# Kernel tuning notes

Hardware: AMD Instinct MI355X
Metric: run time of the kernel (lower is better)

Reference implementation:

```python
import jax, jax.numpy as jnp
import numpy as np

NEG_SLOPE = 0.2
EPS = 1e-16


def gat_conv(x, edge_index, W, att_src, att_dst, bias, heads, out_ch, concat):
    """PyG-style GATConv (eval mode, add_self_loops=True)."""
    N = x.shape[0]
    h = (x @ W).reshape(N, heads, out_ch)              # [N,H,C]
    loop = jnp.arange(N, dtype=edge_index.dtype)
    src = jnp.concatenate([edge_index[0], loop])       # [E+N]
    dst = jnp.concatenate([edge_index[1], loop])
    a_src = jnp.sum(h * att_src, axis=-1)              # [N,H]
    a_dst = jnp.sum(h * att_dst, axis=-1)
    e = jax.nn.leaky_relu(a_src[src] + a_dst[dst], NEG_SLOPE)  # [E+N,H]
    # segment softmax over destination nodes
    m = jax.ops.segment_max(e, dst, num_segments=N)
    e = jnp.exp(e - m[dst])
    s = jax.ops.segment_sum(e, dst, num_segments=N)
    alpha = e / (s[dst] + EPS)                         # [E+N,H]
    msg = h[src] * alpha[..., None]                    # [E+N,H,C]
    out = jax.ops.segment_sum(msg, dst, num_segments=N)  # [N,H,C]
    out = out.reshape(N, heads * out_ch) if concat else out.mean(axis=1)
    return out + bias


def setup_inputs() -> dict:
    key = jax.random.key(0)
    ks = jax.random.split(key, 11)
    N, F, E = 100000, 128, 1600000
    H1, C1 = 4, 16
    H2, C2 = 1, 16
    return {
        "x": jax.random.normal(ks[0], (N, F), dtype=jnp.float32),
        "edge_index": jax.random.randint(ks[1], (2, E), 0, N, dtype=jnp.int64) if jax.config.jax_enable_x64 else jax.random.randint(ks[1], (2, E), 0, N).astype(jnp.int32),
        "W1": jax.random.normal(ks[2], (F, H1 * C1), dtype=jnp.float32) * 0.1,
        "att_src1": jax.random.normal(ks[3], (H1, C1), dtype=jnp.float32) * 0.1,
        "att_dst1": jax.random.normal(ks[4], (H1, C1), dtype=jnp.float32) * 0.1,
        "bias1": jax.random.normal(ks[5], (H1 * C1,), dtype=jnp.float32) * 0.1,
        "W2": jax.random.normal(ks[6], (H1 * C1, H2 * C2), dtype=jnp.float32) * 0.1,
        "att_src2": jax.random.normal(ks[7], (H2, C2), dtype=jnp.float32) * 0.1,
        "att_dst2": jax.random.normal(ks[8], (H2, C2), dtype=jnp.float32) * 0.1,
        "bias2": jax.random.normal(ks[9], (C2,), dtype=jnp.float32) * 0.1,
    }


def reference(x, edge_index, W1, att_src1, att_dst1, bias1, W2, att_src2, att_dst2, bias2):
    # dropout is identity in eval mode
    h = gat_conv(x, edge_index, W1, att_src1, att_dst1, bias1, heads=4, out_ch=16, concat=True)
    h = jax.nn.elu(h)
    h = gat_conv(h, edge_index, W2, att_src2, att_dst2, bias2, heads=1, out_ch=16, concat=False)
    return jax.nn.log_softmax(h, axis=1)
```

## Files before the change

kernel.cpp:

```cpp
#include <hip/hip_runtime.h>
#include <hip/hip_fp16.h>
#include <hip/hip_bf16.h>
#include <math.h>


#define BSH 8
#define BCAP 5120
#define CHK 4096

typedef __attribute__((ext_vector_type(8))) short short8;
typedef __attribute__((ext_vector_type(8))) _Float16 half8;
typedef __attribute__((ext_vector_type(4))) _Float16 half4;
typedef __attribute__((ext_vector_type(4))) float float4v;

static __device__ __forceinline__ short f2bf(float f) {
    __hip_bfloat16 b = __float2bfloat16(f);
    return *reinterpret_cast<short*>(&b);
}

__global__ __launch_bounds__(256) void k_pre(const int* __restrict__ ei, int* __restrict__ cursor,
                                             int* __restrict__ stage, int E, int NBK,
                                             const float* __restrict__ x,
                                             const float* __restrict__ W1,
                                             const float* __restrict__ att_src1,
                                             const float* __restrict__ att_dst1,
                                             __half* __restrict__ h1,
                                             float* __restrict__ a_src, float* __restrict__ a_dst,
                                             int N, int GS) {
    __shared__ __align__(16) char smem[80 * 136 * 2];
    int tid = threadIdx.x;
    if (blockIdx.x < GS) {
        int* hist = (int*)smem;
        int* cnt2 = hist + 512;
        int* base = cnt2 + 512;
        int e0 = blockIdx.x * CHK;
        int nedge = E - e0; if (nedge > CHK) nedge = CHK;
        int nv4 = nedge >> 2, rem = nedge & 3;
        const int4* dv4 = (const int4*)(ei + E + e0);
        const int4* sv4 = (const int4*)(ei + e0);
        for (int i = tid; i < 512; i += 256) { hist[i] = 0; cnt2[i] = 0; }
        __syncthreads();
        for (int i = tid; i < nv4; i += 256) {
            int4 d = dv4[i];
            atomicAdd(&hist[d.x >> BSH], 1);
            atomicAdd(&hist[d.y >> BSH], 1);
            atomicAdd(&hist[d.z >> BSH], 1);
            atomicAdd(&hist[d.w >> BSH], 1);
        }
        if (tid < rem) atomicAdd(&hist[ei[E + e0 + nv4 * 4 + tid] >> BSH], 1);
        __syncthreads();
        for (int b = tid; b < NBK; b += 256) {
            int c = hist[b];
            if (c > 0) base[b] = b * BCAP + atomicAdd(&cursor[b], c);
        }
        __syncthreads();
        for (int i = tid; i < nv4; i += 256) {
            int4 s = sv4[i];
            int4 d = dv4[i];
            int b, r;
            b = d.x >> BSH; r = atomicAdd(&cnt2[b], 1);
            stage[base[b] + r] = s.x | ((d.x & 255) << 17);
            b = d.y >> BSH; r = atomicAdd(&cnt2[b], 1);
            stage[base[b] + r] = s.y | ((d.y & 255) << 17);
            b = d.z >> BSH; r = atomicAdd(&cnt2[b], 1);
            stage[base[b] + r] = s.z | ((d.z & 255) << 17);
            b = d.w >> BSH; r = atomicAdd(&cnt2[b], 1);
            stage[base[b] + r] = s.w | ((d.w & 255) << 17);
        }
        if (tid < rem) {
            int e = nv4 * 4 + tid;
            int s = ei[e0 + e];
            int d = ei[E + e0 + e];
            int b = d >> BSH;
            int r = atomicAdd(&cnt2[b], 1);
            stage[base[b] + r] = s | ((d & 255) << 17);
        }
    } else {
        short* wt = (short*)smem;
        for (int i = tid; i < 128 * 64; i += 256) {
            int k = i >> 6, c = i & 63;
            wt[c * 136 + k] = f2bf(W1[i]);
        }
        for (int i = tid; i < 16 * 128; i += 256) {
            int col = i >> 7, k = i & 127;
            float v = 0.f;
            if (col < 8) {
                int h = col & 3;
                const float* att = (col < 4) ? att_src1 : att_dst1;
                #pragma unroll
                for (int c = 0; c < 16; c++) v += W1[k * 64 + h * 16 + c] * att[h * 16 + c];
            }
            wt[(64 + col) * 136 + k] = f2bf(v);
        }
        __syncthreads();
        int wave = tid >> 6, lane = tid & 63;
        int m = lane & 15, q = lane >> 4;
        int nbase = (blockIdx.x - GS) * 64 + wave * 16;
        int anode = nbase + m;
        bool rowok = anode < N;
        const float* xrow = x + (size_t)(rowok ? anode : 0) * 128 + q * 8;

        float4v acc[5];
        #pragma unroll
        for (int ct = 0; ct < 5; ct++)
            #pragma unroll
            for (int r = 0; r < 4; r++) acc[ct][r] = 0.f;

        #pragma unroll
        for (int kc = 0; kc < 4; kc++) {
            float4 u0 = make_float4(0.f, 0.f, 0.f, 0.f), u1 = u0;
            if (rowok) {
                u0 = *(const float4*)(xrow + kc * 32);
                u1 = *(const float4*)(xrow + kc * 32 + 4);
            }
            short8 af;
            af[0] = f2bf(u0.x); af[1] = f2bf(u0.y); af[2] = f2bf(u0.z); af[3] = f2bf(u0.w);
            af[4] = f2bf(u1.x); af[5] = f2bf(u1.y); af[6] = f2bf(u1.z); af[7] = f2bf(u1.w);
            #pragma unroll
            for (int ct = 0; ct < 5; ct++) {
                short8 bf = *(const short8*)&wt[(ct * 16 + m) * 136 + kc * 32 + q * 8];
                acc[ct] = __builtin_amdgcn_mfma_f32_16x16x32_bf16(af, bf, acc[ct], 0, 0, 0);
            }
        }
        #pragma unroll
        for (int ct = 0; ct < 4; ct++) {
            #pragma unroll
            for (int r = 0; r < 4; r++) {
                int n = nbase + q * 4 + r;
                if (n < N) h1[(size_t)n * 64 + ct * 16 + m] = __float2half(acc[ct][r]);
            }
        }
        #pragma unroll
        for (int r = 0; r < 4; r++) {
            int n = nbase + q * 4 + r;
            if (n < N) {
                float v = acc[4][r];
                if (m < 4) a_src[n * 4 + m] = v;
                else if (m < 8) a_dst[n * 4 + (m - 4)] = v;
            }
        }
    }
}

__global__ __launch_bounds__(256) void k_build2(const int* __restrict__ stage,
                                                const int* __restrict__ cursor,
                                                int* __restrict__ row_start,
                                                int* __restrict__ csr,
                                                int NBK, int E, int N) {
    __shared__ int cnt[128];
    __shared__ int lb[128];
    __shared__ int cur[128];
    __shared__ int sA[256];
    int blk = blockIdx.x, tid = threadIdx.x;
    int b = blk >> 1, half = blk & 1;
    int nodes0 = (b << BSH) + (half << 7);
    int nnodes = N - nodes0;
    if (nnodes > 128) nnodes = 128;
    if (nnodes < 0) nnodes = 0;
    int partial = 0;
    for (int i = tid; i < b; i += 256) partial += cursor[i];
    sA[tid] = partial;
    __syncthreads();
    for (int off = 128; off >= 1; off >>= 1) {
        if (tid < off) sA[tid] += sA[tid + off];
        __syncthreads();
    }
    int ebase = sA[0];
    int ecnt = cursor[b];
    __syncthreads();
    if (b == 0 && half == 0 && tid == 0) row_start[N] = E + N;
    const int* sbk = stage + b * BCAP;
    if (tid < 128) cnt[tid] = (tid < nnodes) ? 1 : 0;
    __syncthreads();
    int hb = half << 7;
    int e4 = ecnt & ~3;
    for (int e = tid * 4; e < e4; e += 1024) {
        int4 v = *(const int4*)&sbk[e];
        int l;
        l = (v.x >> 17) & 255; if ((l & 128) == hb) atomicAdd(&cnt[l & 127], 1);
        l = (v.y >> 17) & 255; if ((l & 128) == hb) atomicAdd(&cnt[l & 127], 1);
        l = (v.z >> 17) & 255; if ((l & 128) == hb) atomicAdd(&cnt[l & 127], 1);
        l = (v.w >> 17) & 255; if ((l & 128) == hb) atomicAdd(&cnt[l & 127], 1);
    }
    if (tid < (ecnt & 3)) {
        int l = (sbk[e4 + tid] >> 17) & 255;
        if ((l & 128) == hb) atomicAdd(&cnt[l & 127], 1);
    }
    __syncthreads();
    int myc = (tid < 128) ? cnt[tid] : 0;
    sA[tid] = myc;
    __syncthreads();
    for (int off = 1; off < 128; off <<= 1) {
        int r = sA[tid] + ((tid >= off) ? sA[tid - off] : 0);
        __syncthreads();
        sA[tid] = r;
        __syncthreads();
    }
    int own_width = sA[127];
    int own_edges = own_width - nnodes;
    int half0_edges = half ? (ecnt - own_edges) : 0;
    int gb = ebase + half0_edges + nodes0;
    if (tid < 128) {
        lb[tid] = sA[tid] - myc;
        cur[tid] = 1;
    }
    __syncthreads();
    if (tid < nnodes) {
        row_start[nodes0 + tid] = gb + lb[tid];
        csr[gb + lb[tid]] = nodes0 + tid;
    }
    __syncthreads();
    for (int e = tid * 4; e < e4; e += 1024) {
        int4 v = *(const int4*)&sbk[e];
        int l, r;
        l = (v.x >> 17) & 255;
        if ((l & 128) == hb) { r = atomicAdd(&cur[l & 127], 1); csr[gb + lb[l & 127] + r] = v.x & 0x1FFFF; }
        l = (v.y >> 17) & 255;
        if ((l & 128) == hb) { r = atomicAdd(&cur[l & 127], 1); csr[gb + lb[l & 127] + r] = v.y & 0x1FFFF; }
        l = (v.z >> 17) & 255;
        if ((l & 128) == hb) { r = atomicAdd(&cur[l & 127], 1); csr[gb + lb[l & 127] + r] = v.z & 0x1FFFF; }
        l = (v.w >> 17) & 255;
        if ((l & 128) == hb) { r = atomicAdd(&cur[l & 127], 1); csr[gb + lb[l & 127] + r] = v.w & 0x1FFFF; }
    }
    if (tid < (ecnt & 3)) {
        int v = sbk[e4 + tid];
        int l = (v >> 17) & 255;
        if ((l & 128) == hb) {
            int r = atomicAdd(&cur[l & 127], 1);
            csr[gb + lb[l & 127] + r] = v & 0x1FFFF;
        }
    }
}

__global__ __launch_bounds__(256) void k_agg1f(const int* __restrict__ row_start,
                                               const int* __restrict__ csr_src,
                                               const float* __restrict__ a_src,
                                               const float* __restrict__ a_dst,
                                               const __half* __restrict__ h1,
                                               const float* __restrict__ bias,
                                               const float* __restrict__ W2,
                                               const float* __restrict__ att_src2,
                                               const float* __restrict__ att_dst2,
                                               __half* __restrict__ h2,
                                               float* __restrict__ a_src2,
                                               float* __restrict__ a_dst2, int N) {
    __shared__ float sW2[64 * 17];
    __shared__ float sAs[16], sAd[16];
    int tid = threadIdx.x;
    for (int i = tid; i < 1024; i += 256) sW2[(i >> 4) * 17 + (i & 15)] = W2[i];
    if (tid < 16) { sAs[tid] = att_src2[tid]; sAd[tid] = att_dst2[tid]; }
    __syncthreads();
    int wave = tid >> 6, lane = tid & 63;
    int grp = lane >> 3, sub = lane & 3, par = (lane >> 2) & 1;
    int node = blockIdx.x * 32 + wave * 8 + grp;
    if (node >= N) return;
    int row = row_start[node];
    int deg = row_start[node + 1] - row;
    float adm = a_dst[node * 4 + sub];
    const _Float16* hb = (const _Float16*)h1 + sub * 16;
    const int* cp = csr_src + row + par;
    float A[16];
    #pragma unroll
    for (int c = 0; c < 16; c++) A[c] = 0.f;
    float sh = 0.f;
    int c0 = 0, c1 = 0, c2 = 0, c3 = 0;
    if (deg >= 8) { c0 = cp[0]; c1 = cp[2]; c2 = cp[4]; c3 = cp[6]; }
    int j = 0;
    for (; j + 8 <= deg; j += 8) {
        int s0 = c0, s1 = c1, s2 = c2, s3 = c3;
        float x0 = a_src[s0 * 4 + sub] + adm;
        float x1 = a_src[s1 * 4 + sub] + adm;
        float x2 = a_src[s2 * 4 + sub] + adm;
        float x3 = a_src[s3 * 4 + sub] + adm;
        half8 p0 = *(const half8*)(hb + (size_t)s0 * 64);
        half8 q0 = *(const half8*)(hb + (size_t)s0 * 64 + 8);
        half8 p1 = *(const half8*)(hb + (size_t)s1 * 64);
        half8 q1 = *(const half8*)(hb + (size_t)s1 * 64 + 8);
        half8 p2 = *(const half8*)(hb + (size_t)s2 * 64);
        half8 q2 = *(const half8*)(hb + (size_t)s2 * 64 + 8);
        half8 p3 = *(const half8*)(hb + (size_t)s3 * 64);
        half8 q3 = *(const half8*)(hb + (size_t)s3 * 64 + 8);
        if (j + 16 <= deg) {
            c0 = cp[j + 8]; c1 = cp[j + 10]; c2 = cp[j + 12]; c3 = cp[j + 14];
        }
        float e0 = __expf(fmaxf(x0, 0.2f * x0));
        float e1 = __expf(fmaxf(x1, 0.2f * x1));
        float e2 = __expf(fmaxf(x2, 0.2f * x2));
        float e3 = __expf(fmaxf(x3, 0.2f * x3));
        sh += (e0 + e1) + (e2 + e3);
        #pragma unroll
        for (int c = 0; c < 8; c++) {
            A[c]     += e0 * (float)p0[c] + e1 * (float)p1[c]
                      + e2 * (float)p2[c] + e3 * (float)p3[c];
            A[c + 8] += e0 * (float)q0[c] + e1 * (float)q1[c]
                      + e2 * (float)q2[c] + e3 * (float)q3[c];
        }
    }
    for (; j < deg; j += 2) {
        int idx = j + par;
        if (idx < deg) {
            int s = csr_src[row + idx];
            float xv = a_src[s * 4 + sub] + adm;
            half8 p = *(const half8*)(hb + (size_t)s * 64);
            half8 q = *(const half8*)(hb + (size_t)s * 64 + 8);
            float e = __expf(fmaxf(xv, 0.2f * xv));
            sh += e;
            #pragma unroll
            for (int c = 0; c < 8; c++) {
                A[c]     += e * (float)p[c];
                A[c + 8] += e * (float)q[c];
            }
        }
    }
    sh += __shfl_xor(sh, 4, 64);
    #pragma unroll
    for (int c = 0; c < 16; c++) A[c] += __shfl_xor(A[c], 4, 64);
    float iv = 1.f / (sh + 1e-16f);
    const float4* bb = (const float4*)bias + sub * 4;
    float o[16];
    #pragma unroll
    for (int c4 = 0; c4 < 4; c4++) {
        float4 b = bb[c4];
        float o0 = A[c4 * 4 + 0] * iv + b.x;
        float o1 = A[c4 * 4 + 1] * iv + b.y;
        float o2 = A[c4 * 4 + 2] * iv + b.z;
        float o3 = A[c4 * 4 + 3] * iv + b.w;
        o[c4 * 4 + 0] = (o0 > 0.f) ? o0 : (__expf(o0) - 1.f);
        o[c4 * 4 + 1] = (o1 > 0.f) ? o1 : (__expf(o1) - 1.f);
        o[c4 * 4 + 2] = (o2 > 0.f) ? o2 : (__expf(o2) - 1.f);
        o[c4 * 4 + 3] = (o3 > 0.f) ? o3 : (__expf(o3) - 1.f);
    }
    float pk[8];
    #pragma unroll
    for (int kk = 0; kk < 8; kk++) pk[kk] = 0.f;
    #pragma unroll
    for (int cc = 0; cc < 16; cc++) {
        float ov = o[cc];
        const float* wr = &sW2[(sub * 16 + cc) * 17 + par * 8];
        #pragma unroll
        for (int kk = 0; kk < 8; kk++) pk[kk] += ov * wr[kk];
    }
    #pragma unroll
    for (int kk = 0; kk < 8; kk++) {
        pk[kk] += __shfl_xor(pk[kk], 1, 64);
        pk[kk] += __shfl_xor(pk[kk], 2, 64);
    }
    if (sub == 0) {
        union { __half2 hh[4]; float4 f; } u;
        u.hh[0] = __floats2half2_rn(pk[0], pk[1]);
        u.hh[1] = __floats2half2_rn(pk[2], pk[3]);
        u.hh[2] = __floats2half2_rn(pk[4], pk[5]);
        u.hh[3] = __floats2half2_rn(pk[6], pk[7]);
        *(float4*)&h2[(size_t)node * 16 + par * 8] = u.f;
    }
    float ps = 0.f, pd = 0.f;
    #pragma unroll
    for (int kk = 0; kk < 8; kk++) {
        ps += pk[kk] * sAs[par * 8 + kk];
        pd += pk[kk] * sAd[par * 8 + kk];
    }
    ps += __shfl_xor(ps, 4, 64);
    pd += __shfl_xor(pd, 4, 64);
    if (sub == 0 && par == 0) { a_src2[node] = ps; a_dst2[node] = pd; }
}

__global__ __launch_bounds__(256) void k_agg2(const int* __restrict__ row_start,
                                              const int* __restrict__ csr_src,
                                              const float* __restrict__ a_src,
                                              const float* __restrict__ a_dst,
                                              const __half* __restrict__ h2,
                                              const float* __restrict__ bias,
                                              float* __restrict__ out, int N) {
    int tid = threadIdx.x;
    int wave = tid >> 6, lane = tid & 63;
    int grp = lane >> 3, sub = lane & 3, par = (lane >> 2) & 1;
    int node = blockIdx.x * 32 + wave * 8 + grp;
    if (node >= N) return;
    int row = row_start[node];
    int deg = row_start[node + 1] - row;
    float ad = a_dst[node];
    const _Float16* hb = (const _Float16*)h2 + sub * 4;
    const int* cp = csr_src + row + par;
    float A0 = 0.f, A1 = 0.f, A2 = 0.f, A3 = 0.f;
    float sh = 0.f;
    int c0 = 0, c1 = 0, c2 = 0, c3 = 0;
    if (deg >= 8) { c0 = cp[0]; c1 = cp[2]; c2 = cp[4]; c3 = cp[6]; }
    int j = 0;
    for (; j + 8 <= deg; j += 8) {
        int s0 = c0, s1 = c1, s2 = c2, s3 = c3;
        float x0 = a_src[s0] + ad;
        float x1 = a_src[s1] + ad;
        float x2 = a_src[s2] + ad;
        float x3 = a_src[s3] + ad;
        half4 v0 = *(const half4*)(hb + (size_t)s0 * 16);
        half4 v1 = *(const half4*)(hb + (size_t)s1 * 16);
        half4 v2 = *(const half4*)(hb + (size_t)s2 * 16);
        half4 v3 = *(const half4*)(hb + (size_t)s3 * 16);
        if (j + 16 <= deg) {
            c0 = cp[j + 8]; c1 = cp[j + 10]; c2 = cp[j + 12]; c3 = cp[j + 14];
        }
        float e0 = __expf(fmaxf(x0, 0.2f * x0));
        float e1 = __expf(fmaxf(x1, 0.2f * x1));
        float e2 = __expf(fmaxf(x2, 0.2f * x2));
        float e3 = __expf(fmaxf(x3, 0.2f * x3));
        sh += (e0 + e1) + (e2 + e3);
        A0 += e0 * (float)v0[0] + e1 * (float)v1[0] + e2 * (float)v2[0] + e3 * (float)v3[0];
        A1 += e0 * (float)v0[1] + e1 * (float)v1[1] + e2 * (float)v2[1] + e3 * (float)v3[1];
        A2 += e0 * (float)v0[2] + e1 * (float)v1[2] + e2 * (float)v2[2] + e3 * (float)v3[2];
        A3 += e0 * (float)v0[3] + e1 * (float)v1[3] + e2 * (float)v2[3] + e3 * (float)v3[3];
    }
    for (; j < deg; j += 2) {
        int idx = j + par;
        if (idx < deg) {
            int s = csr_src[row + idx];
            float xv = a_src[s] + ad;
            half4 v = *(const half4*)(hb + (size_t)s * 16);
            float e = __expf(fmaxf(xv, 0.2f * xv));
            sh += e;
            A0 += e * (float)v[0];
            A1 += e * (float)v[1];
            A2 += e * (float)v[2];
            A3 += e * (float)v[3];
        }
    }
    sh += __shfl_xor(sh, 4, 64);
    A0 += __shfl_xor(A0, 4, 64);
    A1 += __shfl_xor(A1, 4, 64);
    A2 += __shfl_xor(A2, 4, 64);
    A3 += __shfl_xor(A3, 4, 64);
    float iv = 1.f / (sh + 1e-16f);
    float4 b = ((const float4*)bias)[sub];
    float v0 = A0 * iv + b.x;
    float v1 = A1 * iv + b.y;
    float v2 = A2 * iv + b.z;
    float v3 = A3 * iv + b.w;
    float mx = fmaxf(fmaxf(v0, v1), fmaxf(v2, v3));
    mx = fmaxf(mx, __shfl_xor(mx, 1, 64));
    mx = fmaxf(mx, __shfl_xor(mx, 2, 64));
    float se = __expf(v0 - mx) + __expf(v1 - mx) + __expf(v2 - mx) + __expf(v3 - mx);
    se += __shfl_xor(se, 1, 64);
    se += __shfl_xor(se, 2, 64);
    float ls = mx + __logf(se);
    if (par == 0)
        *(float4*)&out[(size_t)node * 16 + sub * 4] =
            make_float4(v0 - ls, v1 - ls, v2 - ls, v3 - ls);
}

extern "C" void kernel_launch(void* const* d_in, const int* in_sizes, int n_in,
                              void* d_out, int out_size, void* d_ws, size_t ws_size,
                              hipStream_t stream) {
    const float* x        = (const float*)d_in[0];
    const int*   ei       = (const int*)d_in[1];
    const float* W1       = (const float*)d_in[2];
    const float* att_src1 = (const float*)d_in[3];
    const float* att_dst1 = (const float*)d_in[4];
    const float* bias1    = (const float*)d_in[5];
    const float* W2       = (const float*)d_in[6];
    const float* att_src2 = (const float*)d_in[7];
    const float* att_dst2 = (const float*)d_in[8];
    const float* bias2    = (const float*)d_in[9];
    float* out = (float*)d_out;

    const int N = in_sizes[0] / 128;
    const int E = in_sizes[1] / 2;
    const int NBK = (N + 255) >> BSH;
    const int GS = (E + CHK - 1) / CHK;
    const int GG = (N + 63) / 64;

    char* p = (char*)d_ws;
    auto alloc = [&](size_t bytes) -> void* {
        void* r = (void*)p;
        p += (bytes + 255) & ~(size_t)255;
        return r;
    };
    __half* h1     = (__half*)alloc((size_t)N * 64 * 2);
    __half* h2     = (__half*)alloc((size_t)N * 16 * 2);
    float* a_src1  = (float*)alloc((size_t)N * 4 * 4);
    float* a_dst1  = (float*)alloc((size_t)N * 4 * 4);
    float* a_src2  = (float*)alloc((size_t)N * 4);
    float* a_dst2  = (float*)alloc((size_t)N * 4);
    int*   row_st  = (int*)alloc((size_t)(N + 1) * 4);
    int*   csr     = (int*)alloc((size_t)(E + N) * 4);
    int*   stage   = (int*)alloc((size_t)NBK * BCAP * 4);
    int*   cursor  = (int*)alloc((size_t)NBK * 4);
    (void)ws_size; (void)n_in; (void)out_size;

    hipMemsetAsync(cursor, 0, (size_t)NBK * 4, stream);
    k_pre<<<GS + GG, 256, 0, stream>>>(ei, cursor, stage, E, NBK,
                                       x, W1, att_src1, att_dst1,
                                       h1, a_src1, a_dst1, N, GS);
    k_build2<<<NBK * 2, 256, 0, stream>>>(stage, cursor, row_st, csr, NBK, E, N);
    k_agg1f<<<(N + 31) / 32, 256, 0, stream>>>(row_st, csr, a_src1, a_dst1, h1, bias1,
                                               W2, att_src2, att_dst2,
                                               h2, a_src2, a_dst2, N);
    k_agg2<<<(N + 31) / 32, 256, 0, stream>>>(row_st, csr, a_src2, a_dst2, h2, bias2, out, N);
}
```

Before: 232.4 us.

## Precompute bf16 weight tile once, widen gather unroll, add occupancy hints

A small init kernel now zeroes the bucket cursors, replacing the memset, and builds the transposed bf16 W1 plus attention-projected columns once in global memory. Each GEMM block in k_pre then copies that tile with vector loads instead of recomputing it per block, which removes redundant W1 reads and dot products. Both aggregation kernels gain an outer loop that handles 16 edges per iteration with 8 independent gathers in flight, to expose more memory-level parallelism. They also add a launch-bounds minimum of 4 blocks; the extra unrolling raises register pressure, which this hint may turn into spills.

```diff
diff --git a/kernel.cpp b/kernel.cpp
--- a/kernel.cpp
+++ b/kernel.cpp
@@ -18,12 +18,37 @@
     return *reinterpret_cast<short*>(&b);
 }
 
+__global__ __launch_bounds__(256) void k_init(int* __restrict__ cursor, int NBK,
+                                              const float* __restrict__ W1,
+                                              const float* __restrict__ att_src1,
+                                              const float* __restrict__ att_dst1,
+                                              short* __restrict__ wtg) {
+    int tid = threadIdx.x;
+    if (blockIdx.x == 0) {
+        for (int i = tid; i < NBK; i += 256) cursor[i] = 0;
+    } else {
+        for (int i = tid; i < 128 * 64; i += 256) {
+            int k = i >> 6, c = i & 63;
+            wtg[c * 136 + k] = f2bf(W1[i]);
+        }
+        for (int i = tid; i < 16 * 128; i += 256) {
+            int col = i >> 7, k = i & 127;
+            float v = 0.f;
+            if (col < 8) {
+                int h = col & 3;
+                const float* att = (col < 4) ? att_src1 : att_dst1;
+                #pragma unroll
+                for (int c = 0; c < 16; c++) v += W1[k * 64 + h * 16 + c] * att[h * 16 + c];
+            }
+            wtg[(64 + col) * 136 + k] = f2bf(v);
+        }
+    }
+}
+
 __global__ __launch_bounds__(256) void k_pre(const int* __restrict__ ei, int* __restrict__ cursor,
                                              int* __restrict__ stage, int E, int NBK,
                                              const float* __restrict__ x,
-                                             const float* __restrict__ W1,
-                                             const float* __restrict__ att_src1,
-                                             const float* __restrict__ att_dst1,
+                                             const short* __restrict__ wtg,
                                              __half* __restrict__ h1,
                                              float* __restrict__ a_src, float* __restrict__ a_dst,
                                              int N, int GS) {
@@ -77,20 +102,10 @@
         }
     } else {
         short* wt = (short*)smem;
-        for (int i = tid; i < 128 * 64; i += 256) {
-            int k = i >> 6, c = i & 63;
-            wt[c * 136 + k] = f2bf(W1[i]);
-        }
-        for (int i = tid; i < 16 * 128; i += 256) {
-            int col = i >> 7, k = i & 127;
-            float v = 0.f;
-            if (col < 8) {
-                int h = col & 3;
-                const float* att = (col < 4) ? att_src1 : att_dst1;
-                #pragma unroll
-                for (int c = 0; c < 16; c++) v += W1[k * 64 + h * 16 + c] * att[h * 16 + c];
-            }
-            wt[(64 + col) * 136 + k] = f2bf(v);
+        {
+            int4* wd = (int4*)wt;
+            const int4* ws = (const int4*)wtg;
+            for (int i = tid; i < (80 * 136 * 2) / 16; i += 256) wd[i] = ws[i];
         }
         __syncthreads();
         int wave = tid >> 6, lane = tid & 63;
@@ -232,7 +247,7 @@
     }
 }
 
-__global__ __launch_bounds__(256) void k_agg1f(const int* __restrict__ row_start,
+__global__ __launch_bounds__(256, 4) void k_agg1f(const int* __restrict__ row_start,
                                                const int* __restrict__ csr_src,
                                                const float* __restrict__ a_src,
                                                const float* __restrict__ a_dst,
@@ -263,11 +278,48 @@
     #pragma unroll
     for (int c = 0; c < 16; c++) A[c] = 0.f;
     float sh = 0.f;
-    int c0 = 0, c1 = 0, c2 = 0, c3 = 0;
-    if (deg >= 8) { c0 = cp[0]; c1 = cp[2]; c2 = cp[4]; c3 = cp[6]; }
     int j = 0;
+    if (deg >= 16) {
+        int c[8];
+        #pragma unroll
+        for (int u = 0; u < 8; u++) c[u] = cp[2 * u];
+        for (; j + 16 <= deg; j += 16) {
+            int s[8];
+            #pragma unroll
+            for (int u = 0; u < 8; u++) s[u] = c[u];
+            float xv[8];
+            #pragma unroll
+            for (int u = 0; u < 8; u++) xv[u] = a_src[s[u] * 4 + sub] + adm;
+            half8 p[8], q[8];
+            #pragma unroll
+            for (int u = 0; u < 8; u++) {
+                p[u] = *(const half8*)(hb + (size_t)s[u] * 64);
+                q[u] = *(const half8*)(hb + (size_t)s[u] * 64 + 8);
+            }
+            if (j + 32 <= deg) {
+                #pragma unroll
+                for (int u = 0; u < 8; u++) c[u] = cp[j + 16 + 2 * u];
+            }
+            float e[8];
+            #pragma unroll
+            for (int u = 0; u < 8; u++) e[u] = __expf(fmaxf(xv[u], 0.2f * xv[u]));
+            #pragma unroll
+            for (int u = 0; u < 8; u++) sh += e[u];
+            #pragma unroll
+            for (int ch = 0; ch < 8; ch++) {
+                float aA = 0.f, aB = 0.f;
+                #pragma unroll
+                for (int u = 0; u < 8; u++) {
+                    aA += e[u] * (float)p[u][ch];
+                    aB += e[u] * (float)q[u][ch];
+                }
+                A[ch] += aA;
+                A[ch + 8] += aB;
+            }
+        }
+    }
     for (; j + 8 <= deg; j += 8) {
-        int s0 = c0, s1 = c1, s2 = c2, s3 = c3;
+        int s0 = cp[j], s1 = cp[j + 2], s2 = cp[j + 4], s3 = cp[j + 6];
         float x0 = a_src[s0 * 4 + sub] + adm;
         float x1 = a_src[s1 * 4 + sub] + adm;
         float x2 = a_src[s2 * 4 + sub] + adm;
@@ -280,9 +332,6 @@
         half8 q2 = *(const half8*)(hb + (size_t)s2 * 64 + 8);
         half8 p3 = *(const half8*)(hb + (size_t)s3 * 64);
         half8 q3 = *(const half8*)(hb + (size_t)s3 * 64 + 8);
-        if (j + 16 <= deg) {
-            c0 = cp[j + 8]; c1 = cp[j + 10]; c2 = cp[j + 12]; c3 = cp[j + 14];
-        }
         float e0 = __expf(fmaxf(x0, 0.2f * x0));
         float e1 = __expf(fmaxf(x1, 0.2f * x1));
         float e2 = __expf(fmaxf(x2, 0.2f * x2));
@@ -364,7 +413,7 @@
     if (sub == 0 && par == 0) { a_src2[node] = ps; a_dst2[node] = pd; }
 }
 
-__global__ __launch_bounds__(256) void k_agg2(const int* __restrict__ row_start,
+__global__ __launch_bounds__(256, 4) void k_agg2(const int* __restrict__ row_start,
                                               const int* __restrict__ csr_src,
                                               const float* __restrict__ a_src,
                                               const float* __restrict__ a_dst,
@@ -383,11 +432,40 @@
     const int* cp = csr_src + row + par;
     float A0 = 0.f, A1 = 0.f, A2 = 0.f, A3 = 0.f;
     float sh = 0.f;
-    int c0 = 0, c1 = 0, c2 = 0, c3 = 0;
-    if (deg >= 8) { c0 = cp[0]; c1 = cp[2]; c2 = cp[4]; c3 = cp[6]; }
     int j = 0;
+    if (deg >= 16) {
+        int c[8];
+        #pragma unroll
+        for (int u = 0; u < 8; u++) c[u] = cp[2 * u];
+        for (; j + 16 <= deg; j += 16) {
+            int s[8];
+            #pragma unroll
+            for (int u = 0; u < 8; u++) s[u] = c[u];
+            float xv[8];
+            #pragma unroll
+            for (int u = 0; u < 8; u++) xv[u] = a_src[s[u]] + ad;
+            half4 v[8];
+            #pragma unroll
+            for (int u = 0; u < 8; u++) v[u] = *(const half4*)(hb + (size_t)s[u] * 16);
+            if (j + 32 <= deg) {
+                #pragma unroll
+                for (int u = 0; u < 8; u++) c[u] = cp[j + 16 + 2 * u];
+            }
+            float e[8];
+            #pragma unroll
+            for (int u = 0; u < 8; u++) e[u] = __expf(fmaxf(xv[u], 0.2f * xv[u]));
+            #pragma unroll
+            for (int u = 0; u < 8; u++) {
+                sh += e[u];
+                A0 += e[u] * (float)v[u][0];
+                A1 += e[u] * (float)v[u][1];
+                A2 += e[u] * (float)v[u][2];
+                A3 += e[u] * (float)v[u][3];
+            }
+        }
+    }
     for (; j + 8 <= deg; j += 8) {
-        int s0 = c0, s1 = c1, s2 = c2, s3 = c3;
+        int s0 = cp[j], s1 = cp[j + 2], s2 = cp[j + 4], s3 = cp[j + 6];
         float x0 = a_src[s0] + ad;
         float x1 = a_src[s1] + ad;
         float x2 = a_src[s2] + ad;
@@ -396,9 +474,6 @@
         half4 v1 = *(const half4*)(hb + (size_t)s1 * 16);
         half4 v2 = *(const half4*)(hb + (size_t)s2 * 16);
         half4 v3 = *(const half4*)(hb + (size_t)s3 * 16);
-        if (j + 16 <= deg) {
-            c0 = cp[j + 8]; c1 = cp[j + 10]; c2 = cp[j + 12]; c3 = cp[j + 14];
-        }
         float e0 = __expf(fmaxf(x0, 0.2f * x0));
         float e1 = __expf(fmaxf(x1, 0.2f * x1));
         float e2 = __expf(fmaxf(x2, 0.2f * x2));
@@ -483,12 +558,12 @@
     int*   csr     = (int*)alloc((size_t)(E + N) * 4);
     int*   stage   = (int*)alloc((size_t)NBK * BCAP * 4);
     int*   cursor  = (int*)alloc((size_t)NBK * 4);
+    short* wtg     = (short*)alloc(80 * 136 * 2);
     (void)ws_size; (void)n_in; (void)out_size;
 
-    hipMemsetAsync(cursor, 0, (size_t)NBK * 4, stream);
+    k_init<<<2, 256, 0, stream>>>(cursor, NBK, W1, att_src1, att_dst1, wtg);
     k_pre<<<GS + GG, 256, 0, stream>>>(ei, cursor, stage, E, NBK,
-                                       x, W1, att_src1, att_dst1,
-                                       h1, a_src1, a_dst1, N, GS);
+                                       x, wtg, h1, a_src1, a_dst1, N, GS);
     k_build2<<<NBK * 2, 256, 0, stream>>>(stage, cursor, row_st, csr, NBK, E, N);
     k_agg1f<<<(N + 31) / 32, 256, 0, stream>>>(row_st, csr, a_src1, a_dst1, h1, bias1,
                                                W2, att_src2, att_dst2,
```

New measurement: 241.4 us. +3.9%, slower.
